# Kernel tuning notes

Measured on AMD Instinct MI355X. Metric: run time of the kernel, lower is better.

## Reference

```python
import jax, jax.numpy as jnp
import numpy as np


def _conv(x, w, b, stride=1):
    # torch Conv2d(kernel=3, padding=1) in NCHW / OIHW layout
    y = jax.lax.conv_general_dilated(x, w, (stride, stride), ((1, 1), (1, 1)),
                                     dimension_numbers=('NCHW', 'OIHW', 'NCHW'))
    return y + b[None, :, None, None]


def _up2(x):
    # nn.Upsample(scale_factor=2, mode='nearest')
    return jnp.repeat(jnp.repeat(x, 2, axis=2), 2, axis=3)


def _decode(z, fc_w, fc_b, w1, b1, w2, b2, w3, b3):
    # ConvDecoderMid: fc -> [B,32,7,7] -> up -> elu(conv) -> up -> elu(conv) -> sigmoid(conv)
    B = z.shape[0]
    h = (z @ fc_w + fc_b).reshape(B, 32, 7, 7)
    h = _up2(h)
    h = jax.nn.elu(_conv(h, w1, b1))
    h = _up2(h)
    h = jax.nn.elu(_conv(h, w2, b2))
    return jax.nn.sigmoid(_conv(h, w3, b3))  # [B,1,28,28]


def setup_inputs() -> dict:
    key = jax.random.key(0)
    B, L, E = 2048, 64, 8
    ks = jax.random.split(key, 16)
    rn = lambda k, s, sc: jax.random.normal(k, s, dtype=jnp.float32) * sc
    p = {}
    p['x'] = jax.random.uniform(ks[0], (B, 1, 28, 28), dtype=jnp.float32)
    p['eps'] = jax.random.normal(ks[1], (B, L), dtype=jnp.float32)
    # ConvEncoder
    p['enc_w1'] = rn(ks[2], (32, 1, 3, 3), 0.3);  p['enc_b1'] = jnp.zeros((32,), jnp.float32)
    p['enc_w2'] = rn(ks[3], (64, 32, 3, 3), 0.06); p['enc_b2'] = jnp.zeros((64,), jnp.float32)
    p['enc_w3'] = rn(ks[4], (128, 64, 3, 3), 0.04); p['enc_b3'] = jnp.zeros((128,), jnp.float32)
    p['w_mu'] = rn(ks[5], (128 * 7 * 7, L), 0.01); p['b_mu'] = jnp.zeros((L,), jnp.float32)
    p['w_lv'] = rn(ks[6], (128 * 7 * 7, L), 0.01); p['b_lv'] = jnp.zeros((L,), jnp.float32)
    # GatingNetwork
    p['g_w1'] = rn(ks[7], (L, 64), 0.1); p['g_b1'] = jnp.zeros((64,), jnp.float32)
    p['g_w2'] = rn(ks[8], (64, 32), 0.1); p['g_b2'] = jnp.zeros((32,), jnp.float32)
    p['g_w3'] = rn(ks[9], (32, E), 0.1); p['g_b3'] = jnp.zeros((E,), jnp.float32)
    # E ConvDecoderMid experts, params stacked on leading expert axis
    p['d_fc_w'] = rn(ks[10], (E, L, 32 * 7 * 7), 0.05); p['d_fc_b'] = jnp.zeros((E, 32 * 7 * 7), jnp.float32)
    p['d_w1'] = rn(ks[11], (E, 64, 32, 3, 3), 0.06); p['d_b1'] = jnp.zeros((E, 64), jnp.float32)
    p['d_w2'] = rn(ks[12], (E, 32, 64, 3, 3), 0.04); p['d_b2'] = jnp.zeros((E, 32), jnp.float32)
    p['d_w3'] = rn(ks[13], (E, 1, 32, 3, 3), 0.06); p['d_b3'] = jnp.zeros((E, 1), jnp.float32)
    return p


def reference(x, eps, enc_w1, enc_b1, enc_w2, enc_b2, enc_w3, enc_b3,
              w_mu, b_mu, w_lv, b_lv,
              g_w1, g_b1, g_w2, g_b2, g_w3, g_b3,
              d_fc_w, d_fc_b, d_w1, d_b1, d_w2, d_b2, d_w3, d_b3):
    B = x.shape[0]
    # encoder: 28 -> 28 -> 14 -> 7
    h = jax.nn.relu(_conv(x, enc_w1, enc_b1))
    h = jax.nn.relu(_conv(h, enc_w2, enc_b2, stride=2))
    h = jax.nn.relu(_conv(h, enc_w3, enc_b3, stride=2))
    h = h.reshape(B, -1)  # [B, 6272]
    mu = h @ w_mu + b_mu
    log_var = h @ w_lv + b_lv
    z = mu + eps * jnp.exp(0.5 * log_var)
    # gating
    g = jax.nn.relu(z @ g_w1 + g_b1)
    g = jax.nn.relu(g @ g_w2 + g_b2)
    expert_probs = jax.nn.softmax(g @ g_w3 + g_b3, axis=-1)
    expert_indices = jnp.argmax(expert_probs, axis=-1)  # [B]
    # run ALL experts on full batch (faithful to original), stack [E,B,1,28,28]
    all_rec = jax.vmap(_decode, in_axes=(None, 0, 0, 0, 0, 0, 0, 0, 0))(
        z, d_fc_w, d_fc_b, d_w1, d_b1, d_w2, d_b2, d_w3, d_b3)
    reconstructed_x = all_rec[expert_indices, jnp.arange(B)]  # [B,1,28,28]
    logits = jnp.log(expert_probs + 1e-8)
    return (reconstructed_x, mu, log_var, logits, expert_probs)
```

## Files before the change

kernel.cpp:

```cpp
#include <hip/hip_runtime.h>
#include <hip/hip_bf16.h>


#define NB 2048

typedef short bf16x8 __attribute__((ext_vector_type(8)));
typedef float f32x4  __attribute__((ext_vector_type(4)));
typedef unsigned u32x4 __attribute__((ext_vector_type(4)));

static constexpr int OFF_RECON  = 0;
static constexpr int OFF_MU     = 1605632;
static constexpr int OFF_LV     = 1736704;
static constexpr int OFF_LOGITS = 1867776;
static constexpr int OFF_PROBS  = 1884160;

static constexpr size_t WS_U    = 0;
static constexpr size_t WS_Z    = 25690112;
static constexpr size_t WS_IDX  = 25821184;
static constexpr size_t WS_WENC = 25821696;
static constexpr size_t W2S_OFF = 0;
static constexpr size_t W3S_OFF = 36864;
static constexpr size_t WFC_OFF = 184320;
static constexpr size_t HFC_OFF = 0;
static constexpr size_t D1O_OFF = 3211264;
static constexpr size_t W1B_OFF = 17000448;
static constexpr size_t WCB_OFF = 17074176;

__device__ __forceinline__ float relu_f(float v) { return v > 0.f ? v : 0.f; }
__device__ __forceinline__ float elu_f(float v)  {
  return __expf(fminf(v, 0.f)) - 1.f + fmaxf(v, 0.f);
}
__device__ __forceinline__ short f2b(float v) {
  __hip_bfloat16 h = __float2bfloat16(v);
  short s; __builtin_memcpy(&s, &h, 2); return s;
}
__device__ __forceinline__ float s2f(short s) {
  unsigned v = ((unsigned)(unsigned short)s) << 16;
  float f; __builtin_memcpy(&f, &v, 4); return f;
}

__global__ __launch_bounds__(256) void k_prep_enc(
    const float* __restrict__ ew2, const float* __restrict__ ew3,
    const float* __restrict__ wmu, const float* __restrict__ wlv,
    unsigned short* __restrict__ w2s, unsigned short* __restrict__ w3s,
    unsigned* __restrict__ wfc)
{
  const int u = blockIdx.x * 256 + threadIdx.x;
  if (u >= 894976) return;
  if (u >= 92160) {
    const int u2 = u - 92160;
    const int kp = u2 >> 8, r = u2 & 255;
    const int n = r >> 1, j = r & 1;
    const int k = kp * 2 + j;
    const float w = (n < 64) ? wmu[k * 64 + n] : wlv[k * 64 + (n - 64)];
    short h = f2b(w);
    short mm = f2b(w - s2f(h));
    wfc[u2] = (unsigned)(unsigned short)h | ((unsigned)(unsigned short)mm << 16);
    return;
  }
  float w; uint2* dst;
  if (u < 18432) {
    int ic = u & 7, oc = (u >> 3) & 63;
    int r = u >> 9;
    int tap = r % 9, chunk = r / 9;
    w = ew2[oc * 288 + (chunk * 8 + ic) * 9 + tap];
    dst = (uint2*)w2s + u;
  } else {
    int u2 = u - 18432;
    int ic = u2 & 7, oc = (u2 >> 3) & 127;
    int r = u2 >> 10;
    int tap = r % 9, chunk = r / 9;
    w = ew3[oc * 576 + (chunk * 8 + ic) * 9 + tap];
    dst = (uint2*)w3s + u2;
  }
  short h = f2b(w);
  short mm = f2b(w - s2f(h));
  uint2 pk;
  pk.x = (unsigned)(unsigned short)h | ((unsigned)(unsigned short)mm << 16);
  pk.y = (unsigned)(unsigned short)h | ((unsigned)(unsigned short)h << 16);
  *dst = pk;
}

__global__ __launch_bounds__(512, 4) void k_conv12(
    const float* __restrict__ x,
    const float* __restrict__ w1, const float* __restrict__ b1,
    const float* __restrict__ b2g, const unsigned short* __restrict__ w2s,
    float* __restrict__ h2f)
{
  __shared__ float sX[900];
  __shared__ float sB2[64];
  __shared__ __align__(16) short sH[900 * 40];

  const int n = blockIdx.x, t = threadIdx.x;

  for (int idx = t; idx < 900; idx += 512) {
    int yy = idx / 30, xx = idx % 30;
    float v = 0.f;
    if (yy >= 1 && yy <= 28 && xx >= 1 && xx <= 28)
      v = x[n * 784 + (yy - 1) * 28 + (xx - 1)];
    sX[idx] = v;
  }
  if (t < 64) sB2[t] = b2g[t];
  for (int bi = t; bi < 116; bi += 512) {
    int p;
    if (bi < 30) p = bi;
    else if (bi < 60) p = 870 + (bi - 30);
    else if (bi < 88) p = (bi - 59) * 30;
    else p = (bi - 87) * 30 + 29;
    unsigned* d = (unsigned*)&sH[p * 40];
    #pragma unroll
    for (int j = 0; j < 20; ++j) d[j] = 0u;
  }
  __syncthreads();

  float xw[2][9];
  int hp[2]; bool pvld[2];
  #pragma unroll
  for (int i = 0; i < 2; ++i) {
    int p = t + 512 * i;
    pvld[i] = (p < 784);
    int yy = pvld[i] ? p / 28 : 0, xx = pvld[i] ? p % 28 : 0;
    hp[i] = (yy + 1) * 30 + xx + 1;
    #pragma unroll
    for (int k = 0; k < 9; ++k)
      xw[i][k] = sX[(yy + k / 3) * 30 + xx + (k % 3)];
  }

  const int lane = t & 63, wv = t >> 6;
  const int q = lane >> 4, m16 = lane & 15;
  const int nth = wv & 1, mh = wv >> 1;
  const int nm = (mh == 0) ? 4 : 3;

  int abase[4];
  #pragma unroll
  for (int mtl = 0; mtl < 4; ++mtl) {
    int m = (mh + 4 * mtl) * 16 + m16; if (m > 195) m = 195;
    int yy = m / 14, xx = m % 14;
    abase[mtl] = (yy * 60 + xx * 2) * 40 + q * 8;
  }
  f32x4 acc[4][2];
  #pragma unroll
  for (int a = 0; a < 4; ++a) { acc[a][0] = (f32x4)0.f; acc[a][1] = (f32x4)0.f; }

  for (int c = 0; c < 4; ++c) {
    #pragma unroll
    for (int o = 0; o < 8; ++o) {
      const int oc = c * 8 + o;
      float wr[9];
      #pragma unroll
      for (int k = 0; k < 9; ++k) wr[k] = w1[oc * 9 + k];
      const float bb = b1[oc];
      #pragma unroll
      for (int i = 0; i < 2; ++i) if (pvld[i]) {
        float v = bb;
        #pragma unroll
        for (int k = 0; k < 9; ++k) v += xw[i][k] * wr[k];
        v = relu_f(v);
        short h = f2b(v); float hf = s2f(h);
        short mm = f2b(v - hf); float mf = s2f(mm);
        short ll = f2b(v - hf - mf);
        uint2 pk;
        pk.x = (unsigned)(unsigned short)h | ((unsigned)(unsigned short)h << 16);
        pk.y = (unsigned)(unsigned short)mm | ((unsigned)(unsigned short)ll << 16);
        *(uint2*)&sH[hp[i] * 40 + o * 4] = pk;
      }
    }
    __syncthreads();

    const unsigned short* wb = w2s + (size_t)c * 18432;
    for (int tap = 0; tap < 9; ++tap) {
      const int toff = ((tap / 3) * 30 + (tap % 3)) * 40;
      bf16x8 A[4];
      #pragma unroll
      for (int mtl = 0; mtl < 4; ++mtl)
        A[mtl] = *(const bf16x8*)&sH[abase[mtl] + toff];
      #pragma unroll
      for (int ntl = 0; ntl < 2; ++ntl) {
        const int ocl = nth * 32 + ntl * 16 + m16;
        bf16x8 B = *(const bf16x8*)&wb[(tap * 64 + ocl) * 32 + q * 8];
        #pragma unroll
        for (int mtl = 0; mtl < 4; ++mtl)
          if (mtl < nm)
            acc[mtl][ntl] = __builtin_amdgcn_mfma_f32_16x16x32_bf16(A[mtl], B, acc[mtl][ntl], 0, 0, 0);
      }
    }
    __syncthreads();
  }

  #pragma unroll
  for (int mtl = 0; mtl < 4; ++mtl) {
    if (mtl < nm) {
      const int mt = mh + 4 * mtl;
      #pragma unroll
      for (int ntl = 0; ntl < 2; ++ntl) {
        const int oc = nth * 32 + ntl * 16 + m16;
        const float bb = sB2[oc];
        #pragma unroll
        for (int r = 0; r < 4; ++r) {
          int p = mt * 16 + q * 4 + r;
          if (p < 196)
            h2f[(size_t)n * 12544 + p * 64 + oc] = relu_f(acc[mtl][ntl][r] + bb);
        }
      }
    }
  }
}

__global__ __launch_bounds__(256, 4) void k_conv3(
    float* hb,
    const unsigned short* __restrict__ w3s,
    const float* __restrict__ b3)
{
  __shared__ __align__(16) short sIn[256 * 40];
  __shared__ float sB3[128];
  const int n = blockIdx.x, t = threadIdx.x;
  if (t < 128) sB3[t] = b3[t];
  for (int bi = t; bi < 60; bi += 256) {
    int p;
    if (bi < 16) p = bi;
    else if (bi < 32) p = 240 + (bi - 16);
    else if (bi < 46) p = (bi - 31) * 16;
    else p = (bi - 45) * 16 + 15;
    unsigned* d = (unsigned*)&sIn[p * 40];
    #pragma unroll
    for (int j = 0; j < 20; ++j) d[j] = 0u;
  }
  const int lane = t & 63, wv = t >> 6;
  const int q = lane >> 4, m16 = lane & 15;
  int abase[4];
  #pragma unroll
  for (int mtl = 0; mtl < 4; ++mtl) {
    int m = mtl * 16 + m16; if (m > 48) m = 48;
    int yy = m / 7, xx = m % 7;
    abase[mtl] = (yy * 32 + xx * 2) * 40 + q * 8;
  }
  f32x4 acc[4][2];
  #pragma unroll
  for (int a = 0; a < 4; ++a) { acc[a][0] = (f32x4)0.f; acc[a][1] = (f32x4)0.f; }
  __syncthreads();

  for (int c = 0; c < 8; ++c) {
    __syncthreads();
    if (t < 196) {
      const int pix = t;
      const int rr = pix / 14 + 1, cc = pix % 14 + 1;
      const float* src = &hb[(size_t)n * 12544 + pix * 64 + c * 8];
      float4 v0 = *(const float4*)src;
      float4 v1 = *(const float4*)(src + 4);
      float vv[8] = {v0.x, v0.y, v0.z, v0.w, v1.x, v1.y, v1.z, v1.w};
      short* drow = &sIn[(rr * 16 + cc) * 40];
      #pragma unroll
      for (int ic = 0; ic < 8; ++ic) {
        float v = vv[ic];
        short h = f2b(v); float hf = s2f(h);
        short mm = f2b(v - hf); float mf = s2f(mm);
        short ll = f2b(v - hf - mf);
        uint2 pk;
        pk.x = (unsigned)(unsigned short)h | ((unsigned)(unsigned short)h << 16);
        pk.y = (unsigned)(unsigned short)mm | ((unsigned)(unsigned short)ll << 16);
        *(uint2*)&drow[ic * 4] = pk;
      }
    }
    __syncthreads();

    const unsigned short* wc = w3s + (size_t)c * 36864;
    for (int tap = 0; tap < 9; ++tap) {
      const int toff = ((tap / 3) * 16 + (tap % 3)) * 40;
      bf16x8 A[4];
      #pragma unroll
      for (int mtl = 0; mtl < 4; ++mtl)
        A[mtl] = *(const bf16x8*)&sIn[abase[mtl] + toff];
      #pragma unroll
      for (int ntl = 0; ntl < 2; ++ntl) {
        const int oc = wv * 32 + ntl * 16 + m16;
        bf16x8 B = *(const bf16x8*)&wc[(tap * 128 + oc) * 32 + q * 8];
        #pragma unroll
        for (int mtl = 0; mtl < 4; ++mtl)
          acc[mtl][ntl] = __builtin_amdgcn_mfma_f32_16x16x32_bf16(A[mtl], B, acc[mtl][ntl], 0, 0, 0);
      }
    }
  }

  unsigned* hbp = (unsigned*)hb;
  #pragma unroll
  for (int mtl = 0; mtl < 4; ++mtl) {
    #pragma unroll
    for (int ntl = 0; ntl < 2; ++ntl) {
      const int oc = wv * 32 + ntl * 16 + m16;
      const float bb = sB3[oc];
      #pragma unroll
      for (int r = 0; r < 4; ++r) {
        int m = mtl * 16 + q * 4 + r;
        if (m < 49) {
          float v = relu_f(acc[mtl][ntl][r] + bb);
          short h = f2b(v);
          short mm = f2b(v - s2f(h));
          hbp[(size_t)n * 12544 + oc * 49 + m] =
              (unsigned)(unsigned short)h | ((unsigned)(unsigned short)mm << 16);
        }
      }
    }
  }
}

__global__ __launch_bounds__(256) void k_fc(
    const unsigned* __restrict__ A2,
    const unsigned* __restrict__ wfc,
    float* __restrict__ Uf)
{
  const int t = threadIdx.x;
  const int lane = t & 63, wv = t >> 6;
  const int q = lane >> 4, m16 = lane & 15;
  const int m0 = blockIdx.x * 64;
  const int s  = blockIdx.y;

  const unsigned* arow[4];
  #pragma unroll
  for (int mt = 0; mt < 4; ++mt)
    arow[mt] = A2 + (size_t)(m0 + mt * 16 + m16) * 12544 + s * 784 + 2 * q;
  const unsigned* brow[2];
  #pragma unroll
  for (int ntl = 0; ntl < 2; ++ntl)
    brow[ntl] = wfc + (size_t)(s * 392 + q) * 256 + ((wv * 2 + ntl) * 16 + m16) * 2;

  f32x4 acc[4][2];
  #pragma unroll
  for (int a = 0; a < 4; ++a) { acc[a][0] = (f32x4)0.f; acc[a][1] = (f32x4)0.f; }

  #pragma unroll 2
  for (int kt = 0; kt < 98; ++kt) {
    bf16x8 Af[4];
    #pragma unroll
    for (int mt = 0; mt < 4; ++mt) {
      uint2 u = *(const uint2*)(arow[mt] + kt * 8);
      u32x4 w = { (u.x << 16) | (u.x & 0xffffu), u.x >> 16,
                  (u.y << 16) | (u.y & 0xffffu), u.y >> 16 };
      Af[mt] = __builtin_bit_cast(bf16x8, w);
    }
    #pragma unroll
    for (int ntl = 0; ntl < 2; ++ntl) {
      uint2 u = *(const uint2*)(brow[ntl] + kt * 1024);
      u32x4 w = { u.x, (u.x << 16) | (u.x & 0xffffu),
                  u.y, (u.y << 16) | (u.y & 0xffffu) };
      bf16x8 Bf = __builtin_bit_cast(bf16x8, w);
      #pragma unroll
      for (int mt = 0; mt < 4; ++mt)
        acc[mt][ntl] = __builtin_amdgcn_mfma_f32_16x16x32_bf16(Af[mt], Bf, acc[mt][ntl], 0, 0, 0);
    }
  }

  #pragma unroll
  for (int mt = 0; mt < 4; ++mt) {
    #pragma unroll
    for (int ntl = 0; ntl < 2; ++ntl) {
      const int n = (wv * 2 + ntl) * 16 + m16;
      #pragma unroll
      for (int r = 0; r < 4; ++r) {
        const int row = m0 + mt * 16 + q * 4 + r;
        Uf[(size_t)row * 12544 + 6272 + s * 128 + n] = acc[mt][ntl][r];
      }
    }
  }
}

__global__ __launch_bounds__(256) void k_gate(
    const float* __restrict__ Ubase,
    const float* __restrict__ b_mu, const float* __restrict__ b_lv,
    const float* __restrict__ eps,
    const float* __restrict__ gw1, const float* __restrict__ gb1,
    const float* __restrict__ gw2, const float* __restrict__ gb2,
    const float* __restrict__ gw3, const float* __restrict__ gb3,
    float* __restrict__ out, float* __restrict__ zbuf, int* __restrict__ idxbuf)
{
  __shared__ float sZ[4][64];
  __shared__ float sG1[4][64];
  __shared__ float sG2[4][32];
  const int t = threadIdx.x;
  const int wv = t >> 6, lane = t & 63;
  const int m = blockIdx.x * 4 + wv;
  const float* __restrict__ Up = Ubase + (size_t)m * 12544 + 6272;

  {
    const int k = lane;
    float mu = b_mu[k], lv = b_lv[k];
    #pragma unroll
    for (int s8 = 0; s8 < 8; ++s8) {
      mu += Up[s8 * 128 + k];
      lv += Up[s8 * 128 + 64 + k];
    }
    out[OFF_MU + m * 64 + k] = mu;
    out[OFF_LV + m * 64 + k] = lv;
    float zz = mu + eps[m * 64 + k] * expf(0.5f * lv);
    sZ[wv][k] = zz;
    zbuf[m * 64 + k] = zz;
  }

  {
    const int j = lane;
    float a = gb1[j];
    for (int k = 0; k < 64; ++k) a += sZ[wv][k] * gw1[k * 64 + j];
    sG1[wv][j] = relu_f(a);
  }
  if (lane < 32) {
    const int j = lane;
    float a = gb2[j];
    for (int k = 0; k < 64; ++k) a += sG1[wv][k] * gw2[k * 32 + j];
    sG2[wv][j] = relu_f(a);
  }
  float l = -1e30f;
  if (lane < 8) {
    float a = gb3[lane];
    for (int k = 0; k < 32; ++k) a += sG2[wv][k] * gw3[k * 8 + lane];
    l = a;
  }
  float mx = l;
  #pragma unroll
  for (int off = 4; off; off >>= 1) mx = fmaxf(mx, __shfl_xor(mx, off, 8));
  float p = expf(l - mx);
  float ssum = p;
  #pragma unroll
  for (int off = 4; off; off >>= 1) ssum += __shfl_xor(ssum, off, 8);
  float pj = p / ssum;
  if (lane < 8) {
    out[OFF_PROBS + m * 8 + lane] = pj;
    out[OFF_LOGITS + m * 8 + lane] = logf(pj + 1e-8f);
  }
  float pmax = pj;
  #pragma unroll
  for (int off = 4; off; off >>= 1) pmax = fmaxf(pmax, __shfl_xor(pmax, off, 8));
  unsigned long long msk = __ballot(lane < 8 && pj == pmax);
  if (lane == 0) idxbuf[m] = __ffsll(msk) - 1;
}

__global__ __launch_bounds__(256) void k_prep(
    const float* __restrict__ dw1, const float* __restrict__ dw2,
    unsigned short* __restrict__ w1b, unsigned short* __restrict__ wcb)
{
  const int e = blockIdx.x, job = blockIdx.y, t = threadIdx.x;
  if (job == 0) {
    for (int idx = t; idx < 18432; idx += 256) {
      int tap = idx >> 11;
      int rem = idx & 2047;
      int octile = rem >> 9;
      int lane = (rem >> 3) & 63;
      int j = idx & 7;
      int oc = octile * 16 + (lane & 15);
      int ic = (lane >> 4) * 8 + j;
      w1b[(size_t)e * 18432 + idx] =
          (unsigned short)f2b(dw1[(size_t)e * 18432 + (oc * 32 + ic) * 9 + tap]);
    }
  } else {
    const int par = job - 1, py = par >> 1, px = par & 1;
    for (int v = t; v < 8192; v += 256) {
      int s = v >> 10;
      int nt = (v >> 9) & 1;
      int lane = (v >> 3) & 63;
      int j = v & 7;
      int oc = nt * 16 + (lane & 15);
      int tap = s >> 1, h = s & 1;
      int ty = tap >> 1, tx = tap & 1;
      int icg = h * 32 + (lane >> 4) * 8 + j;
      int ys = (ty == 0) ? 0 : (1 + py);
      int yc = (ty == py) ? 1 : 2;
      int xs = (tx == 0) ? 0 : (1 + px);
      int xc = (tx == px) ? 1 : 2;
      const float* wp = &dw2[(size_t)e * 18432 + (oc * 64 + icg) * 9];
      float a = 0.f;
      for (int ky = ys; ky < ys + yc; ++ky)
        for (int kx = xs; kx < xs + xc; ++kx)
          a += wp[ky * 3 + kx];
      wcb[((size_t)e * 4 + par) * 8192 + v] = (unsigned short)f2b(a);
    }
  }
}

__global__ __launch_bounds__(256) void k_dfc(
    const float* __restrict__ zbuf, const int* __restrict__ idxbuf,
    const float* __restrict__ fcw, const float* __restrict__ fcb,
    unsigned* __restrict__ hfcb)
{
  __shared__ float sZ[64];
  __shared__ __align__(16) unsigned short sO[1568];
  const int n = blockIdx.x, t = threadIdx.x;
  const int e = idxbuf[n];
  if (t < 64) sZ[t] = zbuf[n * 64 + t];
  __syncthreads();
  const float* __restrict__ W = fcw + (size_t)e * 100352;
  const int i40 = t, i41 = t + 256;
  const bool v1 = (i41 < 392);
  float a0[4], a1[4];
  {
    float4 b0 = *(const float4*)&fcb[e * 1568 + i40 * 4];
    a0[0] = b0.x; a0[1] = b0.y; a0[2] = b0.z; a0[3] = b0.w;
    if (v1) {
      float4 b1v = *(const float4*)&fcb[e * 1568 + i41 * 4];
      a1[0] = b1v.x; a1[1] = b1v.y; a1[2] = b1v.z; a1[3] = b1v.w;
    } else { a1[0] = a1[1] = a1[2] = a1[3] = 0.f; }
  }
  for (int k = 0; k < 64; ++k) {
    const float zk = sZ[k];
    float4 w0 = *(const float4*)&W[k * 1568 + i40 * 4];
    a0[0] += zk * w0.x; a0[1] += zk * w0.y; a0[2] += zk * w0.z; a0[3] += zk * w0.w;
    if (v1) {
      float4 w1v = *(const float4*)&W[k * 1568 + i41 * 4];
      a1[0] += zk * w1v.x; a1[1] += zk * w1v.y; a1[2] += zk * w1v.z; a1[3] += zk * w1v.w;
    }
  }
  #pragma unroll
  for (int c = 0; c < 4; ++c) {
    int j = i40 * 4 + c;
    int ic = j / 49, p = j % 49;
    sO[p * 32 + ic] = (unsigned short)f2b(a0[c]);
  }
  if (v1) {
    #pragma unroll
    for (int c = 0; c < 4; ++c) {
      int j = i41 * 4 + c;
      int ic = j / 49, p = j % 49;
      sO[p * 32 + ic] = (unsigned short)f2b(a1[c]);
    }
  }
  __syncthreads();
  for (int idx = t; idx < 784; idx += 256)
    hfcb[(size_t)n * 784 + idx] = ((const unsigned*)sO)[idx];
}

__global__ __launch_bounds__(256) void k_d1(
    const unsigned* __restrict__ hfcb, const int* __restrict__ idxbuf,
    const unsigned* __restrict__ w1b, const float* __restrict__ b,
    __hip_bfloat16* __restrict__ d1o)
{
  __shared__ __align__(16) short sIn[256 * 40];
  __shared__ __align__(16) short sW[9 * 64 * 32];
  __shared__ float sB[64];

  const int n = blockIdx.x, t = threadIdx.x;
  const int e = idxbuf[n];

  {
    int r = t >> 4, c = t & 15;
    bool inter = (r >= 1 && r <= 14 && c >= 1 && c <= 14);
    int src = inter ? (((r - 1) >> 1) * 7 + ((c - 1) >> 1)) : 0;
    const unsigned* hp = &hfcb[(size_t)n * 784 + src * 16];
    unsigned* dst = (unsigned*)&sIn[t * 40];
    #pragma unroll
    for (int i = 0; i < 16; ++i) dst[i] = inter ? hp[i] : 0u;
  }
  {
    const unsigned* wsrc = w1b + (size_t)e * 9216;
    unsigned* wd = (unsigned*)sW;
    for (int idx = t; idx < 9216; idx += 256) wd[idx] = wsrc[idx];
  }
  if (t < 64) sB[t] = b[e * 64 + t];
  __syncthreads();

  const int wv = t >> 6, lane = t & 63;
  const int q = lane >> 4, m16 = lane & 15;
  const int ocl = wv * 16 + m16;

  f32x4 acc[13];
  int abase[13];
  #pragma unroll
  for (int mt = 0; mt < 13; ++mt) {
    acc[mt] = (f32x4)0.f;
    int p = mt * 16 + m16; if (p > 195) p = 195;
    int y = p / 14, x = p % 14;
    abase[mt] = (y * 16 + x) * 40 + q * 8;
  }

  for (int tap = 0; tap < 9; ++tap) {
    const int ky = tap / 3, kx = tap % 3;
    const int toff = (ky * 16 + kx) * 40;
    bf16x8 bfrag = *(const bf16x8*)&sW[tap * 2048 + wv * 512 + lane * 8];
    #pragma unroll
    for (int mt = 0; mt < 13; ++mt) {
      bf16x8 afrag = *(const bf16x8*)&sIn[abase[mt] + toff];
      acc[mt] = __builtin_amdgcn_mfma_f32_16x16x32_bf16(afrag, bfrag, acc[mt], 0, 0, 0);
    }
  }

  const float bias = sB[ocl];
  #pragma unroll
  for (int mt = 0; mt < 13; ++mt) {
    #pragma unroll
    for (int r = 0; r < 4; ++r) {
      int p = mt * 16 + q * 4 + r;
      if (p < 196) {
        float v = elu_f(acc[mt][r] + bias);
        short s = f2b(v);
        __builtin_memcpy(&d1o[(size_t)n * 12544 + p * 64 + ocl], &s, 2);
      }
    }
  }
}

__global__ __launch_bounds__(512, 4) void k_d23(
    const unsigned* __restrict__ d1u,
    const int* __restrict__ idxbuf,
    const unsigned* __restrict__ wcb,
    const float* __restrict__ b2,
    const float* __restrict__ w3, const float* __restrict__ b3,
    float* __restrict__ out)
{
  __shared__ __align__(16) short sD1[256 * 72];
  __shared__ __align__(16) short sU[8192];
  __shared__ __align__(16) short sW3b[512];
  __shared__ float sC[196 * 9];
  __shared__ float sB2[32];

  const int n = blockIdx.x, t = threadIdx.x;
  const int e = idxbuf[n];

  {
    int cell = t >> 1, half = t & 1;
    int r = cell >> 4, c = cell & 15;
    bool inter = (r >= 1 && r <= 14 && c >= 1 && c <= 14);
    int src = inter ? ((r - 1) * 14 + (c - 1)) : 0;
    const unsigned* hp = &d1u[(size_t)n * 6272 + src * 32 + half * 16];
    unsigned* dst = (unsigned*)sD1 + cell * 36 + half * 16;
    #pragma unroll
    for (int i = 0; i < 16; ++i) dst[i] = inter ? hp[i] : 0u;
  }
  {
    int nn = t >> 5, k = t & 31;
    if (t < 512) sW3b[t] = (nn < 9) ? f2b(w3[e * 288 + k * 9 + nn]) : (short)0;
  }
  if (t < 32) sB2[t] = b2[e * 32 + t];
  __syncthreads();

  const int wv = t >> 6, lane = t & 63;
  const int q = lane >> 4, m16 = lane & 15;
  const int nt = wv & 1, mh = wv >> 1;
  const int ocl = nt * 16 + m16;
  const int nm = (mh == 0) ? 4 : 3;

  const bf16x8 b3f = *(const bf16x8*)&sW3b[m16 * 32 + q * 8];

  int mt3[2], ab3[2];
  const int nmt3 = (wv < 5) ? 2 : 1;
  #pragma unroll
  for (int i = 0; i < 2; ++i) {
    int mt = wv + 8 * i; if (mt > 12) mt = 12;
    mt3[i] = mt;
    int p = mt * 16 + m16; if (p > 195) p = 195;
    ab3[i] = p * 40 + q * 8;
  }

  int PY[2], PX[2];
  #pragma unroll
  for (int g = 0; g < 2; ++g) {
    int P = t + 512 * g;
    PY[g] = (P < 784) ? P / 28 : -100;
    PX[g] = (P < 784) ? P % 28 : 0;
  }
  float racc[2] = {0.f, 0.f};

  int ab0[4];
  #pragma unroll
  for (int im = 0; im < 4; ++im) {
    int mt = mh + 4 * im;
    int p = mt * 16 + m16; if (p > 195) p = 195;
    int a = p / 14, bb = p % 14;
    ab0[im] = (a * 16 + bb) * 72 + q * 8;
  }

  for (int par = 0; par < 4; ++par) {
    const int py = par >> 1, px = par & 1;

    {
      const unsigned* wc = wcb + ((size_t)e * 4 + par) * 4096;
      unsigned* du = (unsigned*)sU;
      for (int v = t; v < 4096; v += 512) du[v] = wc[v];
    }
    __syncthreads();

    f32x4 acc[4];
    #pragma unroll
    for (int im = 0; im < 4; ++im) acc[im] = (f32x4)0.f;
    const int pbase = (py * 16 + px) * 72;
    for (int s = 0; s < 8; ++s) {
      int tap = s >> 1, h = s & 1;
      int ty = tap >> 1, tx = tap & 1;
      int toff = pbase + (ty * 16 + tx) * 72 + h * 32;
      bf16x8 bfrag = *(const bf16x8*)&sU[s * 1024 + nt * 512 + lane * 8];
      #pragma unroll
      for (int im = 0; im < 4; ++im) {
        if (im < nm) {
          bf16x8 afrag = *(const bf16x8*)&sD1[ab0[im] + toff];
          acc[im] = __builtin_amdgcn_mfma_f32_16x16x32_bf16(afrag, bfrag, acc[im], 0, 0, 0);
        }
      }
    }
    __syncthreads();

    {
      const float bias = sB2[ocl];
      #pragma unroll
      for (int im = 0; im < 4; ++im) {
        if (im < nm) {
          int mt = mh + 4 * im;
          #pragma unroll
          for (int r = 0; r < 4; ++r) {
            int p = mt * 16 + q * 4 + r;
            if (p < 196) sU[p * 40 + ocl] = f2b(elu_f(acc[im][r] + bias));
          }
        }
      }
    }
    __syncthreads();

    #pragma unroll
    for (int i = 0; i < 2; ++i) {
      if (i < nmt3) {
        bf16x8 af = *(const bf16x8*)&sU[ab3[i]];
        f32x4 a3 = (f32x4)0.f;
        a3 = __builtin_amdgcn_mfma_f32_16x16x32_bf16(af, b3f, a3, 0, 0, 0);
        if (m16 < 9) {
          #pragma unroll
          for (int r = 0; r < 4; ++r) {
            int p = mt3[i] * 16 + q * 4 + r;
            if (p < 196) sC[p * 9 + m16] = a3[r];
          }
        }
      }
    }
    __syncthreads();

    #pragma unroll
    for (int g = 0; g < 2; ++g) {
      const int Y = PY[g], X = PX[g];
      if (Y < 0) continue;
      int RS[2]; int nr = 0;
      if ((Y & 1) == py) { RS[0] = Y; nr = 1; }
      else { if (Y > 0) RS[nr++] = Y - 1; if (Y < 27) RS[nr++] = Y + 1; }
      int CS[2]; int nc = 0;
      if ((X & 1) == px) { CS[0] = X; nc = 1; }
      else { if (X > 0) CS[nc++] = X - 1; if (X < 27) CS[nc++] = X + 1; }
      float s = 0.f;
      for (int ir = 0; ir < nr; ++ir) {
        const int R = RS[ir];
        const int a = (R - py) >> 1, ky = R - Y + 1;
        for (int jc = 0; jc < nc; ++jc) {
          const int C = CS[jc];
          const int bq = (C - px) >> 1, kx = C - X + 1;
          s += sC[(a * 14 + bq) * 9 + ky * 3 + kx];
        }
      }
      racc[g] += s;
    }
    __syncthreads();
  }

  const float b3e = b3[e];
  #pragma unroll
  for (int g = 0; g < 2; ++g) {
    int P = t + 512 * g;
    if (P < 784)
      out[OFF_RECON + (size_t)n * 784 + P] = 1.f / (1.f + __expf(-(racc[g] + b3e)));
  }
}

extern "C" void kernel_launch(void* const* d_in, const int* in_sizes, int n_in,
                              void* d_out, int out_size, void* d_ws, size_t ws_size,
                              hipStream_t stream) {
  const float* x    = (const float*)d_in[0];
  const float* eps  = (const float*)d_in[1];
  const float* ew1  = (const float*)d_in[2];
  const float* eb1  = (const float*)d_in[3];
  const float* ew2  = (const float*)d_in[4];
  const float* eb2  = (const float*)d_in[5];
  const float* ew3  = (const float*)d_in[6];
  const float* eb3  = (const float*)d_in[7];
  const float* wmu  = (const float*)d_in[8];
  const float* bmu  = (const float*)d_in[9];
  const float* wlv  = (const float*)d_in[10];
  const float* blv  = (const float*)d_in[11];
  const float* gw1  = (const float*)d_in[12];
  const float* gb1  = (const float*)d_in[13];
  const float* gw2  = (const float*)d_in[14];
  const float* gb2  = (const float*)d_in[15];
  const float* gw3  = (const float*)d_in[16];
  const float* gb3  = (const float*)d_in[17];
  const float* dfcw = (const float*)d_in[18];
  const float* dfcb = (const float*)d_in[19];
  const float* dw1  = (const float*)d_in[20];
  const float* db1  = (const float*)d_in[21];
  const float* dw2  = (const float*)d_in[22];
  const float* db2  = (const float*)d_in[23];
  const float* dw3  = (const float*)d_in[24];
  const float* db3  = (const float*)d_in[25];

  float* out = (float*)d_out;
  float* ws  = (float*)d_ws;

  float* U    = ws + WS_U;
  float* zb   = ws + WS_Z;
  int*   idx  = (int*)(ws + WS_IDX);
  unsigned* hfcb = (unsigned*)(U + HFC_OFF);
  __hip_bfloat16* d1o = (__hip_bfloat16*)(U + D1O_OFF);
  unsigned short* w1b = (unsigned short*)(U + W1B_OFF);
  unsigned short* wcb = (unsigned short*)(U + WCB_OFF);
  unsigned short* w2s = (unsigned short*)(ws + WS_WENC + W2S_OFF);
  unsigned short* w3s = (unsigned short*)(ws + WS_WENC + W3S_OFF);
  unsigned* wfc = (unsigned*)(ws + WS_WENC + WFC_OFF);

  k_prep_enc<<<3496, 256, 0, stream>>>(ew2, ew3, wmu, wlv, w2s, w3s, wfc);
  k_conv12<<<NB, 512, 0, stream>>>(x, ew1, eb1, eb2, w2s, U);
  k_conv3 <<<NB, 256, 0, stream>>>(U, w3s, eb3);
  k_fc    <<<dim3(32, 8), 256, 0, stream>>>((const unsigned*)U, wfc, U);
  k_gate  <<<512, 256, 0, stream>>>(U, bmu, blv, eps, gw1, gb1, gw2, gb2, gw3, gb3,
                                    out, zb, idx);
  k_prep  <<<dim3(8, 5), 256, 0, stream>>>(dw1, dw2, w1b, wcb);
  k_dfc   <<<NB, 256, 0, stream>>>(zb, idx, dfcw, dfcb, hfcb);
  k_d1    <<<NB, 256, 0, stream>>>(hfcb, idx, (const unsigned*)w1b, db1, d1o);
  k_d23   <<<NB, 512, 0, stream>>>((const unsigned*)d1o, idx, (const unsigned*)wcb,
                                   db2, dw3, db3, out);
}
```

Baseline: 566.6 us.

## Fuse encoder conv3 into conv1/conv2 kernel, keeping intermediate in shared memory

Result: faster. 549.6 us (-3.0%).

```diff
diff --git a/kernel.cpp b/kernel.cpp
--- a/kernel.cpp
+++ b/kernel.cpp
@@ -37,6 +37,11 @@
 __device__ __forceinline__ float s2f(short s) {
   unsigned v = ((unsigned)(unsigned short)s) << 16;
   float f; __builtin_memcpy(&f, &v, 4); return f;
+}
+__device__ __forceinline__ unsigned pack2(float v) {
+  short h = f2b(v);
+  short m = f2b(v - s2f(h));
+  return (unsigned)(unsigned short)h | ((unsigned)(unsigned short)m << 16);
 }
 
 __global__ __launch_bounds__(256) void k_prep_enc(
@@ -81,15 +86,17 @@
   *dst = pk;
 }
 
-__global__ __launch_bounds__(512, 4) void k_conv12(
+__global__ __launch_bounds__(512, 4) void k_enc(
     const float* __restrict__ x,
     const float* __restrict__ w1, const float* __restrict__ b1,
     const float* __restrict__ b2g, const unsigned short* __restrict__ w2s,
-    float* __restrict__ h2f)
+    const unsigned short* __restrict__ w3s, const float* __restrict__ b3,
+    unsigned* __restrict__ hb)
 {
   __shared__ float sX[900];
   __shared__ float sB2[64];
-  __shared__ __align__(16) short sH[900 * 40];
+  __shared__ float sB3[128];
+  __shared__ __align__(16) short sH[36000];
 
   const int n = blockIdx.x, t = threadIdx.x;
 
@@ -101,6 +108,7 @@
     sX[idx] = v;
   }
   if (t < 64) sB2[t] = b2g[t];
+  if (t >= 64 && t < 192) sB3[t - 64] = b3[t - 64];
   for (int bi = t; bi < 116; bi += 512) {
     int p;
     if (bi < 30) p = bi;
@@ -187,6 +195,8 @@
     __syncthreads();
   }
 
+  unsigned* h2p = (unsigned*)sH;
+  short* sIn = sH + 25600;
   #pragma unroll
   for (int mtl = 0; mtl < 4; ++mtl) {
     if (mtl < nm) {
@@ -199,23 +209,12 @@
         for (int r = 0; r < 4; ++r) {
           int p = mt * 16 + q * 4 + r;
           if (p < 196)
-            h2f[(size_t)n * 12544 + p * 64 + oc] = relu_f(acc[mtl][ntl][r] + bb);
+            h2p[p * 65 + oc] = pack2(relu_f(acc[mtl][ntl][r] + bb));
         }
       }
     }
   }
-}
-
-__global__ __launch_bounds__(256, 4) void k_conv3(
-    float* hb,
-    const unsigned short* __restrict__ w3s,
-    const float* __restrict__ b3)
-{
-  __shared__ __align__(16) short sIn[256 * 40];
-  __shared__ float sB3[128];
-  const int n = blockIdx.x, t = threadIdx.x;
-  if (t < 128) sB3[t] = b3[t];
-  for (int bi = t; bi < 60; bi += 256) {
+  for (int bi = t; bi < 60; bi += 512) {
     int p;
     if (bi < 16) p = bi;
     else if (bi < 32) p = 240 + (bi - 16);
@@ -225,40 +224,32 @@
     #pragma unroll
     for (int j = 0; j < 20; ++j) d[j] = 0u;
   }
-  const int lane = t & 63, wv = t >> 6;
-  const int q = lane >> 4, m16 = lane & 15;
-  int abase[4];
+
+  const int oc3 = wv * 16 + m16;
+  int abase3[4];
   #pragma unroll
   for (int mtl = 0; mtl < 4; ++mtl) {
     int m = mtl * 16 + m16; if (m > 48) m = 48;
     int yy = m / 7, xx = m % 7;
-    abase[mtl] = (yy * 32 + xx * 2) * 40 + q * 8;
-  }
-  f32x4 acc[4][2];
-  #pragma unroll
-  for (int a = 0; a < 4; ++a) { acc[a][0] = (f32x4)0.f; acc[a][1] = (f32x4)0.f; }
-  __syncthreads();
+    abase3[mtl] = (yy * 32 + xx * 2) * 40 + q * 8;
+  }
+  f32x4 acc3[4];
+  #pragma unroll
+  for (int a = 0; a < 4; ++a) acc3[a] = (f32x4)0.f;
 
   for (int c = 0; c < 8; ++c) {
     __syncthreads();
-    if (t < 196) {
-      const int pix = t;
-      const int rr = pix / 14 + 1, cc = pix % 14 + 1;
-      const float* src = &hb[(size_t)n * 12544 + pix * 64 + c * 8];
-      float4 v0 = *(const float4*)src;
-      float4 v1 = *(const float4*)(src + 4);
-      float vv[8] = {v0.x, v0.y, v0.z, v0.w, v1.x, v1.y, v1.z, v1.w};
-      short* drow = &sIn[(rr * 16 + cc) * 40];
-      #pragma unroll
-      for (int ic = 0; ic < 8; ++ic) {
-        float v = vv[ic];
-        short h = f2b(v); float hf = s2f(h);
-        short mm = f2b(v - hf); float mf = s2f(mm);
-        short ll = f2b(v - hf - mf);
+    if (t < 392) {
+      int pix = t >> 1, icoff = (t & 1) * 4;
+      int rr = pix / 14 + 1, cc = pix % 14 + 1;
+      short* drow = &sIn[(rr * 16 + cc) * 40 + icoff * 4];
+      #pragma unroll
+      for (int i = 0; i < 4; ++i) {
+        unsigned u = h2p[pix * 65 + c * 8 + icoff + i];
         uint2 pk;
-        pk.x = (unsigned)(unsigned short)h | ((unsigned)(unsigned short)h << 16);
-        pk.y = (unsigned)(unsigned short)mm | ((unsigned)(unsigned short)ll << 16);
-        *(uint2*)&drow[ic * 4] = pk;
+        pk.x = (u << 16) | (u & 0xffffu);
+        pk.y = u >> 16;
+        *(uint2*)&drow[i * 4] = pk;
       }
     }
     __syncthreads();
@@ -266,39 +257,23 @@
     const unsigned short* wc = w3s + (size_t)c * 36864;
     for (int tap = 0; tap < 9; ++tap) {
       const int toff = ((tap / 3) * 16 + (tap % 3)) * 40;
-      bf16x8 A[4];
-      #pragma unroll
-      for (int mtl = 0; mtl < 4; ++mtl)
-        A[mtl] = *(const bf16x8*)&sIn[abase[mtl] + toff];
-      #pragma unroll
-      for (int ntl = 0; ntl < 2; ++ntl) {
-        const int oc = wv * 32 + ntl * 16 + m16;
-        bf16x8 B = *(const bf16x8*)&wc[(tap * 128 + oc) * 32 + q * 8];
-        #pragma unroll
-        for (int mtl = 0; mtl < 4; ++mtl)
-          acc[mtl][ntl] = __builtin_amdgcn_mfma_f32_16x16x32_bf16(A[mtl], B, acc[mtl][ntl], 0, 0, 0);
-      }
-    }
-  }
-
-  unsigned* hbp = (unsigned*)hb;
+      bf16x8 B = *(const bf16x8*)&wc[(tap * 128 + oc3) * 32 + q * 8];
+      #pragma unroll
+      for (int mtl = 0; mtl < 4; ++mtl) {
+        bf16x8 A = *(const bf16x8*)&sIn[abase3[mtl] + toff];
+        acc3[mtl] = __builtin_amdgcn_mfma_f32_16x16x32_bf16(A, B, acc3[mtl], 0, 0, 0);
+      }
+    }
+  }
+
+  const float bb3 = sB3[oc3];
   #pragma unroll
   for (int mtl = 0; mtl < 4; ++mtl) {
     #pragma unroll
-    for (int ntl = 0; ntl < 2; ++ntl) {
-      const int oc = wv * 32 + ntl * 16 + m16;
-      const float bb = sB3[oc];
-      #pragma unroll
-      for (int r = 0; r < 4; ++r) {
-        int m = mtl * 16 + q * 4 + r;
-        if (m < 49) {
-          float v = relu_f(acc[mtl][ntl][r] + bb);
-          short h = f2b(v);
-          short mm = f2b(v - s2f(h));
-          hbp[(size_t)n * 12544 + oc * 49 + m] =
-              (unsigned)(unsigned short)h | ((unsigned)(unsigned short)mm << 16);
-        }
-      }
+    for (int r = 0; r < 4; ++r) {
+      int m = mtl * 16 + q * 4 + r;
+      if (m < 49)
+        hb[(size_t)n * 12544 + oc3 * 49 + m] = pack2(relu_f(acc3[mtl][r] + bb3));
     }
   }
 }
@@ -805,8 +780,7 @@
   unsigned* wfc = (unsigned*)(ws + WS_WENC + WFC_OFF);
 
   k_prep_enc<<<3496, 256, 0, stream>>>(ew2, ew3, wmu, wlv, w2s, w3s, wfc);
-  k_conv12<<<NB, 512, 0, stream>>>(x, ew1, eb1, eb2, w2s, U);
-  k_conv3 <<<NB, 256, 0, stream>>>(U, w3s, eb3);
+  k_enc   <<<NB, 512, 0, stream>>>(x, ew1, eb1, eb2, w2s, w3s, eb3, (unsigned*)U);
   k_fc    <<<dim3(32, 8), 256, 0, stream>>>((const unsigned*)U, wfc, U);
   k_gate  <<<512, 256, 0, stream>>>(U, bmu, blv, eps, gw1, gb1, gw2, gb2, gw3, gb3,
                                     out, zb, idx);
```
